# Optimization experiments

Measured on AMD Instinct MI355X. Metric: run time of the kernel, lower is better.

## Reference

```python
import jax, jax.numpy as jnp
from jax import lax
import numpy as np

# LeNet-5 C3 sparse connectivity table (which S2 maps feed each C3 map)
IDX3 = np.array([[0,1,2],[1,2,3],[2,3,4],[3,4,5],[0,4,5],[0,1,5]])            # maps 0-5 (3 inputs)
IDX4 = np.array([[0,1,2,3],[1,2,3,4],[2,3,4,5],[0,3,4,5],[0,1,4,5],
                 [0,1,2,5],[0,1,3,4],[1,2,4,5],[0,2,3,5]])                    # maps 6-14 (4 inputs)


def _conv(x, w):
    return lax.conv_general_dilated(x, w, (1, 1), 'VALID',
                                    dimension_numbers=('NCHW', 'OIHW', 'NCHW'))


def _avgpool2(x):
    s = lax.reduce_window(x, 0.0, lax.add, (1, 1, 2, 2), (1, 1, 2, 2), 'VALID')
    return s * 0.25


def setup_inputs() -> dict:
    key = jax.random.key(0)
    ks = jax.random.split(key, 12)
    f = lambda k, shp: (jax.random.normal(k, shp, dtype=jnp.float32) * 0.1)
    return {
        'x':     jax.random.normal(ks[0], (8192, 1, 32, 32), dtype=jnp.float32),
        'c1_w':  f(ks[1], (6, 1, 5, 5)),   'c1_b': f(ks[2], (6,)),
        'c3_w3': f(ks[3], (6, 3, 5, 5)),   'c3_b3': f(ks[4], (6,)),
        'c3_w4': f(ks[5], (9, 4, 5, 5)),   'c3_b4': f(ks[6], (9,)),
        'c3_w6': f(ks[7], (1, 6, 5, 5)),   'c3_b6': f(ks[8], (1,)),
        'c5_w':  f(ks[9], (120, 16, 5, 5)), 'c5_b': f(ks[10], (120,)),
        'l1_w':  f(ks[11], (84, 120)), 'l1_b': jnp.zeros((84,), jnp.float32),
        'l2_w':  f(jax.random.fold_in(key, 99), (10, 84)), 'l2_b': jnp.zeros((10,), jnp.float32),
    }


def reference(x, c1_w, c1_b, c3_w3, c3_b3, c3_w4, c3_b4, c3_w6, c3_b6,
              c5_w, c5_b, l1_w, l1_b, l2_w, l2_b):
    # C1 + tanh + S2: [B,1,32,32] -> [B,6,14,14]
    out = jnp.tanh(_conv(x, c1_w) + c1_b[None, :, None, None])
    out = _avgpool2(out)

    # C3: fuse the 16 sparse-connectivity convs into one [16,6,5,5] conv
    # by scattering the small per-map kernels into a zero-padded weight.
    W = jnp.zeros((16, 6, 5, 5), dtype=out.dtype)
    W = W.at[np.arange(6)[:, None], IDX3].set(c3_w3)
    W = W.at[np.arange(6, 15)[:, None], IDX4].set(c3_w4)
    W = W.at[15].set(c3_w6[0])
    b = jnp.concatenate([c3_b3, c3_b4, c3_b6])
    out = _conv(out, W) + b[None, :, None, None]          # [B,16,10,10]

    out = _avgpool2(jnp.tanh(out))                        # [B,16,5,5]
    out = _conv(out, c5_w) + c5_b[None, :, None, None]    # [B,120,1,1]
    out = jnp.tanh(out[:, :, 0, 0])                       # [B,120]
    out = jnp.tanh(out @ l1_w.T + l1_b)                   # [B,84]
    return out @ l2_w.T + l2_b                            # [B,10]
```

## Files before the change

kernel.cpp:

```cpp
#include <hip/hip_runtime.h>

typedef float v2f   __attribute__((ext_vector_type(2)));
typedef float f32x4 __attribute__((ext_vector_type(4)));
typedef _Float16 h16;
typedef h16 half8 __attribute__((ext_vector_type(8)));
typedef h16 half4 __attribute__((ext_vector_type(4)));

__device__ __forceinline__ float fast_tanh(float x) {
    float e = __expf(2.0f * x);
    return fmaf(-2.0f, __builtin_amdgcn_rcpf(e + 1.0f), 1.0f);
}
__device__ __forceinline__ half8 cvt8(float4 u0, float4 u1) {
    return (half8){(h16)u0.x,(h16)u0.y,(h16)u0.z,(h16)u0.w,
                   (h16)u1.x,(h16)u1.y,(h16)u1.z,(h16)u1.w};
}

#define S2IMGH 1576

#define C1_IMG 8
#define XROW  40
#define XIMGH (32 * XROW + 8)

__global__ __launch_bounds__(256) void k_c1(
    const float* __restrict__ x, const float* __restrict__ c1_w,
    const float* __restrict__ c1_b, h16* __restrict__ s2g, int B)
{
    __shared__ __align__(16) h16 xs[C1_IMG * XIMGH];
    __shared__ float c1w_s[152];
    __shared__ float c1b_s[8];

    const int tid  = threadIdx.x;
    const int img0 = blockIdx.x * C1_IMG;
    const int nimg = min(C1_IMG, B - img0);
    if (nimg <= 0) return;

    if (tid < 150) c1w_s[tid] = c1_w[tid];
    if (tid < 6)   c1b_s[tid] = c1_b[tid];

    {
        const float4* xg = (const float4*)(x + (size_t)img0 * 1024);
        const int n4 = nimg * 256;
        for (int i = tid; i < n4; i += 256) {
            float4 v = xg[i];
            int img = i >> 8, q = i & 255;
            int row = q >> 3, col4 = (q & 7) << 2;
            *(half4*)(xs + img * XIMGH + row * XROW + col4) =
                (half4){(h16)v.x, (h16)v.y, (h16)v.z, (h16)v.w};
        }
    }
    __syncthreads();

    const int lane = tid & 63, wv = tid >> 6;
    const int nloc = lane & 15, q4 = lane >> 4;

    half8 bf[3][5];
    float bias[3];
    #pragma unroll
    for (int t = 0; t < 3; ++t) {
        const int tile = 3 * wv + t;
        const int map  = tile >> 1;
        const int j    = ((tile & 1) << 4) + nloc;
        bias[t] = c1b_s[map];
        #pragma unroll
        for (int ks = 0; ks < 5; ++ks) {
            half8 f;
            #pragma unroll
            for (int jj = 0; jj < 8; ++jj) {
                const int d = q4 * 8 + jj - j;
                f[jj] = (d >= 0 && d < 5) ? (h16)c1w_s[map * 25 + ks * 5 + d] : (h16)0;
            }
            bf[t][ks] = f;
        }
    }

    const int imgL = nloc >> 1, hf = nloc & 1;
    const h16* xrow = xs + imgL * XIMGH + hf * (14 * XROW) + q4 * 8;
    half8 rf[5];
    #pragma unroll
    for (int r = 0; r < 5; ++r) rf[r] = *(const half8*)(xrow + r * XROW);

    float t0[3][4];
    for (int cr = 0; cr < 14; ++cr) {
        f32x4 acc[3];
        #pragma unroll
        for (int t = 0; t < 3; ++t) acc[t] = (f32x4){0.f, 0.f, 0.f, 0.f};
        #pragma unroll
        for (int ks = 0; ks < 5; ++ks) {
            #pragma unroll
            for (int t = 0; t < 3; ++t)
                acc[t] = __builtin_amdgcn_mfma_f32_16x16x32_f16(rf[ks], bf[t][ks], acc[t], 0, 0, 0);
        }
        if ((cr & 1) == 0) {
            #pragma unroll
            for (int t = 0; t < 3; ++t)
                #pragma unroll
                for (int r = 0; r < 4; ++r)
                    t0[t][r] = fast_tanh(acc[t][r] + bias[t]);
        } else {
            #pragma unroll
            for (int t = 0; t < 3; ++t) {
                const int tile = 3 * wv + t;
                const int jp   = (((tile & 1) << 4) + nloc) >> 1;
                const int map  = tile >> 1;
                #pragma unroll
                for (int r = 0; r < 4; ++r) {
                    float s = t0[t][r] + fast_tanh(acc[t][r] + bias[t]);
                    float o = 0.25f * (s + __shfl_xor(s, 1));
                    const int m = q4 * 4 + r;
                    const int img = m >> 1, mh = m & 1;
                    const int ip  = (cr >> 1) + 7 * mh;
                    if (!(lane & 1) && jp < 14 && img < nimg)
                        s2g[(size_t)(img0 + img) * S2IMGH + (ip * 14 + jp) * 8 + map] = (h16)o;
                }
            }
        }
        if (cr < 13) {
            rf[0] = rf[1]; rf[1] = rf[2]; rf[2] = rf[3]; rf[3] = rf[4];
            rf[4] = *(const half8*)(xrow + (cr + 5) * XROW);
        }
    }
}

#define C3B_HALVES 3584

__device__ __constant__ int C3_INV[16][6] = {
    {0,1,2,-1,-1,-1},{-1,0,1,2,-1,-1},{-1,-1,0,1,2,-1},{-1,-1,-1,0,1,2},
    {0,-1,-1,-1,1,2},{0,1,-1,-1,-1,2},
    {0,1,2,3,-1,-1},{-1,0,1,2,3,-1},{-1,-1,0,1,2,3},{0,-1,-1,1,2,3},
    {0,1,-1,-1,2,3},{0,1,2,-1,-1,3},{0,1,-1,2,3,-1},{-1,0,1,-1,2,3},
    {0,-1,1,2,-1,3},
    {0,1,2,3,4,5}
};

#define K2_SMEM_BYTES (16 * S2IMGH * 2 + C3B_HALVES * 2 + 64)

__global__ __launch_bounds__(256) void k_c3(
    const h16* __restrict__ s2g,
    const float* __restrict__ c3_w3, const float* __restrict__ c3_b3,
    const float* __restrict__ c3_w4, const float* __restrict__ c3_b4,
    const float* __restrict__ c3_w6, const float* __restrict__ c3_b6,
    h16* __restrict__ s4g, int B)
{
    __shared__ __align__(16) char smem[K2_SMEM_BYTES];
    h16*   s2i   = (h16*)smem;
    h16*   c3Bh  = (h16*)(smem + 16 * S2IMGH * 2);
    float* c3b_s = (float*)(smem + 16 * S2IMGH * 2 + C3B_HALVES * 2);

    const int tid  = threadIdx.x;
    const int img0 = blockIdx.x * 16;
    const int nimg = min(16, B - img0);
    if (nimg <= 0) return;

    {
        const int img = tid >> 4;
        if (img < nimg) {
            for (int c = (tid & 15); c < 197; c += 16)
                *(half8*)(s2i + img * S2IMGH + c * 8) =
                    *(const half8*)(s2g + (size_t)(img0 + img) * S2IMGH + c * 8);
        }
    }
    #pragma unroll
    for (int u = 0; u < 14; ++u) {
        const int e = tid + 256 * u;
        const int t = e >> 9, rem = e & 511, L = rem >> 3, c = rem & 7;
        const int n = L & 15, chunk = L >> 4;
        int dr, dc; bool valid = true;
        if (t <= 4)      { dr = chunk; dc = t; }
        else if (t == 5) { dr = 4; dc = chunk; }
        else             { dr = 4; dc = 4; valid = (chunk == 0); }
        float val = 0.0f;
        if (valid && c < 6) {
            const int cc = C3_INV[n][c];
            if (cc >= 0) {
                const int off = dr * 5 + dc;
                if (n < 6)       val = c3_w3[(n * 3 + cc) * 25 + off];
                else if (n < 15) val = c3_w4[((n - 6) * 4 + cc) * 25 + off];
                else             val = c3_w6[cc * 25 + off];
            }
        }
        c3Bh[e] = (h16)val;
    }
    if (tid < 6)        c3b_s[tid] = c3_b3[tid];
    else if (tid < 15)  c3b_s[tid] = c3_b4[tid - 6];
    else if (tid == 15) c3b_s[15]  = c3_b6[0];
    __syncthreads();

    {
        const int lane = tid & 63, wv = tid >> 6;
        const int nloc = lane & 15, q4 = lane >> 4;
        half8 bf[7];
        #pragma unroll
        for (int t = 0; t < 7; ++t)
            bf[t] = *(const half8*)(c3Bh + t * 512 + lane * 8);
        const float bias = c3b_s[nloc];
        const int abase = nloc * S2IMGH;
        for (int q = wv; q < 25; q += 4) {
            const int pr = q / 5, pc = q % 5;
            f32x4 acc[2][2];
            #pragma unroll
            for (int a = 0; a < 2; ++a)
                #pragma unroll
                for (int b2 = 0; b2 < 2; ++b2)
                    acc[a][b2] = (f32x4){0.f, 0.f, 0.f, 0.f};
            #pragma unroll
            for (int a = 0; a < 2; ++a) {
                #pragma unroll
                for (int b2 = 0; b2 < 2; ++b2) {
                    const int r = 2 * pr + a, col = 2 * pc + b2;
                    #pragma unroll
                    for (int t = 0; t < 5; ++t) {
                        half8 A = *(const half8*)(s2i + abase + ((r + q4) * 14 + col + t) * 8);
                        acc[a][b2] = __builtin_amdgcn_mfma_f32_16x16x32_f16(A, bf[t], acc[a][b2], 0, 0, 0);
                    }
                    half8 A5 = *(const half8*)(s2i + abase + ((r + 4) * 14 + col + q4) * 8);
                    acc[a][b2] = __builtin_amdgcn_mfma_f32_16x16x32_f16(A5, bf[5], acc[a][b2], 0, 0, 0);
                    half8 A6 = *(const half8*)(s2i + abase + ((r + 4) * 14 + col + 4) * 8);
                    acc[a][b2] = __builtin_amdgcn_mfma_f32_16x16x32_f16(A6, bf[6], acc[a][b2], 0, 0, 0);
                }
            }
            const int pos = pr * 5 + pc;
            #pragma unroll
            for (int rr = 0; rr < 4; ++rr) {
                const int img = q4 * 4 + rr;
                if (img < nimg) {
                    float s = fast_tanh(acc[0][0][rr] + bias) + fast_tanh(acc[0][1][rr] + bias)
                            + fast_tanh(acc[1][0][rr] + bias) + fast_tanh(acc[1][1][rr] + bias);
                    s4g[(size_t)(img0 + img) * 400 + nloc * 25 + pos] = (h16)(0.25f * s);
                }
            }
        }
    }
}

#define KT_IMG   16
#define S4L_STR  424
#define C5O_STR  136
#define F6L_STR  104
#define KT_S4L   0
#define KT_C5OL  (KT_IMG * S4L_STR * 2)
#define KT_F6L   (KT_C5OL + KT_IMG * C5O_STR * 2)
#define KT_BIAS  (KT_F6L + KT_IMG * F6L_STR * 2)
#define KT_SMEM  (KT_BIAS + 240 * 4)

__global__ __launch_bounds__(256) void k_tail(
    const h16* __restrict__ s4g,
    const float* __restrict__ c5_w, const float* __restrict__ c5_b,
    const float* __restrict__ l1_w, const float* __restrict__ l1_b,
    const float* __restrict__ l2_w, const float* __restrict__ l2_b,
    float* __restrict__ out, int B)
{
    __shared__ __align__(16) char smem[KT_SMEM];
    h16*   s4l   = (h16*)(smem + KT_S4L);
    h16*   c5ol  = (h16*)(smem + KT_C5OL);
    h16*   f6l   = (h16*)(smem + KT_F6L);
    float* c5b_s = (float*)(smem + KT_BIAS);
    float* l1b_s = c5b_s + 128;
    float* l2b_s = l1b_s + 96;

    const int tid  = threadIdx.x;
    const int img0 = blockIdx.x * KT_IMG;
    const int nimg = min(KT_IMG, B - img0);
    if (nimg <= 0) return;

    if (tid < 128)      c5b_s[tid] = (tid < 120) ? c5_b[tid] : 0.f;
    else if (tid < 224) { int i = tid - 128; l1b_s[i] = (i < 84) ? l1_b[i] : 0.f; }
    else if (tid < 240) { int i = tid - 224; l2b_s[i] = (i < 10) ? l2_b[i] : 0.f; }

    {
        const half8 z = {(h16)0,(h16)0,(h16)0,(h16)0,(h16)0,(h16)0,(h16)0,(h16)0};
        for (int i = tid; i < KT_IMG * 53; i += 256) {
            int img = i / 53, cc = i % 53;
            half8 v = z;
            if (img < nimg && cc < 50)
                v = *(const half8*)(s4g + (size_t)(img0 + img) * 400 + cc * 8);
            *(half8*)(s4l + img * S4L_STR + cc * 8) = v;
        }
    }
    __syncthreads();

    const int lane = tid & 63, wv = tid >> 6;
    const int nloc = lane & 15, q4 = lane >> 4;
    const half8 z8 = {(h16)0,(h16)0,(h16)0,(h16)0,(h16)0,(h16)0,(h16)0,(h16)0};

    {
        const int nb = wv * 2;
        f32x4 acc[2];
        acc[0] = (f32x4){0.f,0.f,0.f,0.f};
        acc[1] = (f32x4){0.f,0.f,0.f,0.f};
        for (int ks = 0; ks < 13; ++ks) {
            const int ka = ks * 32 + q4 * 8;
            half8 A = *(const half8*)(s4l + nloc * S4L_STR + ka);
            #pragma unroll
            for (int t = 0; t < 2; ++t) {
                const int n = (nb + t) * 16 + nloc;
                half8 Bf = z8;
                if (n < 120 && ka < 400) {
                    float4 u0 = *(const float4*)(c5_w + n * 400 + ka);
                    float4 u1 = *(const float4*)(c5_w + n * 400 + ka + 4);
                    Bf = cvt8(u0, u1);
                }
                acc[t] = __builtin_amdgcn_mfma_f32_16x16x32_f16(A, Bf, acc[t], 0, 0, 0);
            }
        }
        #pragma unroll
        for (int t = 0; t < 2; ++t) {
            const int o = (nb + t) * 16 + nloc;
            const float bo = c5b_s[o];
            #pragma unroll
            for (int r = 0; r < 4; ++r) {
                const int img = q4 * 4 + r;
                c5ol[img * C5O_STR + o] = (h16)fast_tanh(acc[t][r] + bo);
            }
        }
    }
    __syncthreads();

    if (wv < 3) {
        const int nb = wv * 2;
        f32x4 acc[2];
        acc[0] = (f32x4){0.f,0.f,0.f,0.f};
        acc[1] = (f32x4){0.f,0.f,0.f,0.f};
        for (int ks = 0; ks < 4; ++ks) {
            const int ka = ks * 32 + q4 * 8;
            half8 A = *(const half8*)(c5ol + nloc * C5O_STR + ka);
            #pragma unroll
            for (int t = 0; t < 2; ++t) {
                const int n = (nb + t) * 16 + nloc;
                half8 Bf = z8;
                if (n < 84 && ka < 120) {
                    float4 u0 = *(const float4*)(l1_w + n * 120 + ka);
                    float4 u1 = *(const float4*)(l1_w + n * 120 + ka + 4);
                    Bf = cvt8(u0, u1);
                }
                acc[t] = __builtin_amdgcn_mfma_f32_16x16x32_f16(A, Bf, acc[t], 0, 0, 0);
            }
        }
        #pragma unroll
        for (int t = 0; t < 2; ++t) {
            const int o = (nb + t) * 16 + nloc;
            const float bo = l1b_s[o];
            #pragma unroll
            for (int r = 0; r < 4; ++r) {
                const int img = q4 * 4 + r;
                f6l[img * F6L_STR + o] = (h16)fast_tanh(acc[t][r] + bo);
            }
        }
    }
    __syncthreads();

    if (wv == 0) {
        f32x4 acc = (f32x4){0.f,0.f,0.f,0.f};
        #pragma unroll
        for (int ks = 0; ks < 3; ++ks) {
            const int ka = ks * 32 + q4 * 8;
            half8 A = *(const half8*)(f6l + nloc * F6L_STR + ka);
            half8 Bf = z8;
            #pragma unroll
            for (int i = 0; i < 8; ++i) {
                const int k = ka + i;
                if (nloc < 10 && k < 84) Bf[i] = (h16)l2_w[nloc * 84 + k];
            }
            acc = __builtin_amdgcn_mfma_f32_16x16x32_f16(A, Bf, acc, 0, 0, 0);
        }
        if (nloc < 10) {
            #pragma unroll
            for (int r = 0; r < 4; ++r) {
                const int img = q4 * 4 + r;
                if (img < nimg)
                    out[(size_t)(img0 + img) * 10 + nloc] = acc[r] + l2b_s[nloc];
            }
        }
    }
}

extern "C" void kernel_launch(void* const* d_in, const int* in_sizes, int n_in,
                              void* d_out, int out_size, void* d_ws, size_t ws_size,
                              hipStream_t stream) {
    const float* x     = (const float*)d_in[0];
    const float* c1_w  = (const float*)d_in[1];
    const float* c1_b  = (const float*)d_in[2];
    const float* c3_w3 = (const float*)d_in[3];
    const float* c3_b3 = (const float*)d_in[4];
    const float* c3_w4 = (const float*)d_in[5];
    const float* c3_b4 = (const float*)d_in[6];
    const float* c3_w6 = (const float*)d_in[7];
    const float* c3_b6 = (const float*)d_in[8];
    const float* c5_w  = (const float*)d_in[9];
    const float* c5_b  = (const float*)d_in[10];
    const float* l1_w  = (const float*)d_in[11];
    const float* l1_b  = (const float*)d_in[12];
    const float* l2_w  = (const float*)d_in[13];
    const float* l2_b  = (const float*)d_in[14];
    float* out = (float*)d_out;

    const int B = in_sizes[0] / 1024;

    h16* s2g = (h16*)d_ws;
    h16* s4g = (h16*)((char*)d_ws + (size_t)B * S2IMGH * 2);

    k_c1<<<(B + C1_IMG - 1) / C1_IMG, 256, 0, stream>>>(x, c1_w, c1_b, s2g, B);
    k_c3<<<(B + 15) / 16, 256, 0, stream>>>(s2g, c3_w3, c3_b3, c3_w4, c3_b4,
                                            c3_w6, c3_b6, s4g, B);
    k_tail<<<(B + KT_IMG - 1) / KT_IMG, 256, 0, stream>>>(s4g, c5_w, c5_b,
                                                          l1_w, l1_b, l2_w, l2_b, out, B);
}
```

Before: 178.6 us.

## Load C1 input directly from global and stage S2 output in LDS

k_c1 no longer stages the fp32 input image in shared memory as fp16. Each lane now reads its rows straight from global memory and converts them in registers. S2 results are written to a zero-initialised LDS tile and then copied to global as coalesced 16-byte stores, replacing the earlier scattered 2-byte global writes. k_c3 builds its B-fragment weights and bias directly in registers from global memory instead of going through an LDS table, and zero-fills padding images instead of skipping them. The aim is fewer scattered global stores and fewer LDS round trips, at the cost of redundant uncoalesced global reads of the input and weights.

Measured after the change: 191.2 us. 1.07x slower.

```diff
diff --git a/kernel.cpp b/kernel.cpp
--- a/kernel.cpp
+++ b/kernel.cpp
@@ -1,10 +1,8 @@
 #include <hip/hip_runtime.h>
 
-typedef float v2f   __attribute__((ext_vector_type(2)));
 typedef float f32x4 __attribute__((ext_vector_type(4)));
 typedef _Float16 h16;
 typedef h16 half8 __attribute__((ext_vector_type(8)));
-typedef h16 half4 __attribute__((ext_vector_type(4)));
 
 __device__ __forceinline__ float fast_tanh(float x) {
     float e = __expf(2.0f * x);
@@ -18,14 +16,12 @@
 #define S2IMGH 1576
 
 #define C1_IMG 8
-#define XROW  40
-#define XIMGH (32 * XROW + 8)
 
 __global__ __launch_bounds__(256) void k_c1(
     const float* __restrict__ x, const float* __restrict__ c1_w,
     const float* __restrict__ c1_b, h16* __restrict__ s2g, int B)
 {
-    __shared__ __align__(16) h16 xs[C1_IMG * XIMGH];
+    __shared__ __align__(16) h16 s2l[C1_IMG * S2IMGH];
     __shared__ float c1w_s[152];
     __shared__ float c1b_s[8];
 
@@ -36,17 +32,10 @@
 
     if (tid < 150) c1w_s[tid] = c1_w[tid];
     if (tid < 6)   c1b_s[tid] = c1_b[tid];
-
-    {
-        const float4* xg = (const float4*)(x + (size_t)img0 * 1024);
-        const int n4 = nimg * 256;
-        for (int i = tid; i < n4; i += 256) {
-            float4 v = xg[i];
-            int img = i >> 8, q = i & 255;
-            int row = q >> 3, col4 = (q & 7) << 2;
-            *(half4*)(xs + img * XIMGH + row * XROW + col4) =
-                (half4){(h16)v.x, (h16)v.y, (h16)v.z, (h16)v.w};
-        }
+    {
+        const half8 z = {(h16)0,(h16)0,(h16)0,(h16)0,(h16)0,(h16)0,(h16)0,(h16)0};
+        half8* zp = (half8*)s2l;
+        for (int i = tid; i < C1_IMG * 197; i += 256) zp[i] = z;
     }
     __syncthreads();
 
@@ -74,10 +63,12 @@
     }
 
     const int imgL = nloc >> 1, hf = nloc & 1;
-    const h16* xrow = xs + imgL * XIMGH + hf * (14 * XROW) + q4 * 8;
+    const int imgC = min(imgL, nimg - 1);
+    const float* xg = x + (size_t)(img0 + imgC) * 1024 + hf * (14 * 32) + q4 * 8;
     half8 rf[5];
     #pragma unroll
-    for (int r = 0; r < 5; ++r) rf[r] = *(const half8*)(xrow + r * XROW);
+    for (int r = 0; r < 5; ++r)
+        rf[r] = cvt8(*(const float4*)(xg + r * 32), *(const float4*)(xg + r * 32 + 4));
 
     float t0[3][4];
     for (int cr = 0; cr < 14; ++cr) {
@@ -109,19 +100,26 @@
                     const int m = q4 * 4 + r;
                     const int img = m >> 1, mh = m & 1;
                     const int ip  = (cr >> 1) + 7 * mh;
-                    if (!(lane & 1) && jp < 14 && img < nimg)
-                        s2g[(size_t)(img0 + img) * S2IMGH + (ip * 14 + jp) * 8 + map] = (h16)o;
+                    if (!(lane & 1) && jp < 14)
+                        s2l[img * S2IMGH + (ip * 14 + jp) * 8 + map] = (h16)o;
                 }
             }
         }
         if (cr < 13) {
             rf[0] = rf[1]; rf[1] = rf[2]; rf[2] = rf[3]; rf[3] = rf[4];
-            rf[4] = *(const half8*)(xrow + (cr + 5) * XROW);
-        }
-    }
-}
-
-#define C3B_HALVES 3584
+            rf[4] = cvt8(*(const float4*)(xg + (cr + 5) * 32),
+                         *(const float4*)(xg + (cr + 5) * 32 + 4));
+        }
+    }
+    __syncthreads();
+
+    for (int i = tid; i < C1_IMG * 197; i += 256) {
+        const int img = i / 197, c = i % 197;
+        if (img < nimg)
+            *(half8*)(s2g + (size_t)(img0 + img) * S2IMGH + c * 8) =
+                *(const half8*)(s2l + img * S2IMGH + c * 8);
+    }
+}
 
 __device__ __constant__ int C3_INV[16][6] = {
     {0,1,2,-1,-1,-1},{-1,0,1,2,-1,-1},{-1,-1,0,1,2,-1},{-1,-1,-1,0,1,2},
@@ -132,8 +130,6 @@
     {0,1,2,3,4,5}
 };
 
-#define K2_SMEM_BYTES (16 * S2IMGH * 2 + C3B_HALVES * 2 + 64)
-
 __global__ __launch_bounds__(256) void k_c3(
     const h16* __restrict__ s2g,
     const float* __restrict__ c3_w3, const float* __restrict__ c3_b3,
@@ -141,10 +137,7 @@
     const float* __restrict__ c3_w6, const float* __restrict__ c3_b6,
     h16* __restrict__ s4g, int B)
 {
-    __shared__ __align__(16) char smem[K2_SMEM_BYTES];
-    h16*   s2i   = (h16*)smem;
-    h16*   c3Bh  = (h16*)(smem + 16 * S2IMGH * 2);
-    float* c3b_s = (float*)(smem + 16 * S2IMGH * 2 + C3B_HALVES * 2);
+    __shared__ __align__(16) h16 s2i[16 * S2IMGH];
 
     const int tid  = threadIdx.x;
     const int img0 = blockIdx.x * 16;
@@ -152,47 +145,46 @@
     if (nimg <= 0) return;
 
     {
+        const half8 z = {(h16)0,(h16)0,(h16)0,(h16)0,(h16)0,(h16)0,(h16)0,(h16)0};
         const int img = tid >> 4;
-        if (img < nimg) {
-            for (int c = (tid & 15); c < 197; c += 16)
-                *(half8*)(s2i + img * S2IMGH + c * 8) =
-                    *(const half8*)(s2g + (size_t)(img0 + img) * S2IMGH + c * 8);
-        }
-    }
+        for (int c = (tid & 15); c < 197; c += 16)
+            *(half8*)(s2i + img * S2IMGH + c * 8) =
+                (img < nimg) ? *(const half8*)(s2g + (size_t)(img0 + img) * S2IMGH + c * 8)
+                             : z;
+    }
+
+    const int lane = tid & 63, wv = tid >> 6;
+    const int nloc = lane & 15, q4 = lane >> 4;
+
+    half8 bf[7];
     #pragma unroll
-    for (int u = 0; u < 14; ++u) {
-        const int e = tid + 256 * u;
-        const int t = e >> 9, rem = e & 511, L = rem >> 3, c = rem & 7;
-        const int n = L & 15, chunk = L >> 4;
+    for (int t = 0; t < 7; ++t) {
+        half8 f;
         int dr, dc; bool valid = true;
-        if (t <= 4)      { dr = chunk; dc = t; }
-        else if (t == 5) { dr = 4; dc = chunk; }
-        else             { dr = 4; dc = 4; valid = (chunk == 0); }
-        float val = 0.0f;
-        if (valid && c < 6) {
-            const int cc = C3_INV[n][c];
-            if (cc >= 0) {
-                const int off = dr * 5 + dc;
-                if (n < 6)       val = c3_w3[(n * 3 + cc) * 25 + off];
-                else if (n < 15) val = c3_w4[((n - 6) * 4 + cc) * 25 + off];
-                else             val = c3_w6[cc * 25 + off];
-            }
-        }
-        c3Bh[e] = (h16)val;
-    }
-    if (tid < 6)        c3b_s[tid] = c3_b3[tid];
-    else if (tid < 15)  c3b_s[tid] = c3_b4[tid - 6];
-    else if (tid == 15) c3b_s[15]  = c3_b6[0];
-    __syncthreads();
-
-    {
-        const int lane = tid & 63, wv = tid >> 6;
-        const int nloc = lane & 15, q4 = lane >> 4;
-        half8 bf[7];
-        #pragma unroll
-        for (int t = 0; t < 7; ++t)
-            bf[t] = *(const half8*)(c3Bh + t * 512 + lane * 8);
-        const float bias = c3b_s[nloc];
+        if (t <= 4)      { dr = q4; dc = t; }
+        else if (t == 5) { dr = 4; dc = q4; }
+        else             { dr = 4; dc = 4; valid = (q4 == 0); }
+        #pragma unroll
+        for (int j = 0; j < 8; ++j) {
+            float val = 0.0f;
+            if (valid && j < 6) {
+                const int cc = C3_INV[nloc][j];
+                if (cc >= 0) {
+                    const int off = dr * 5 + dc;
+                    if (nloc < 6)       val = c3_w3[(nloc * 3 + cc) * 25 + off];
+                    else if (nloc < 15) val = c3_w4[((nloc - 6) * 4 + cc) * 25 + off];
+                    else                val = c3_w6[cc * 25 + off];
+                }
+            }
+            f[j] = (h16)val;
+        }
+        bf[t] = f;
+    }
+    const float bias = (nloc < 6) ? c3_b3[nloc]
+                     : (nloc < 15) ? c3_b4[nloc - 6] : c3_b6[0];
+    __syncthreads();
+
+    {
         const int abase = nloc * S2IMGH;
         for (int q = wv; q < 25; q += 4) {
             const int pr = q / 5, pc = q % 5;
```
